# Kernel tuning notes

Measured on AMD Instinct MI355X. Metric: run time of the kernel, lower is better.

Reference implementation:

```python
import jax, jax.numpy as jnp
import numpy as np

B, T, N, F, D, E = 8, 256, 118, 3, 128, 372
G = B * T  # number of graphs after flattening batch*time


def _gcn(x, src, dst, W, b):
    # x: [G, N, Fin] -> PyG GCNConv: X' = D^-1/2 (A+I) D^-1/2 (X W) + b
    h = x @ W  # [G, N, Fout]
    deg = jnp.ones((N,), h.dtype).at[dst].add(1.0)  # in-degree + self loop
    inv = deg ** -0.5
    norm = inv[src] * inv[dst]  # [E]
    agg = h * (1.0 / deg)[None, :, None]  # self-loop term: inv[i]*inv[i] = 1/deg
    agg = agg.at[:, dst].add(h[:, src] * norm[None, :, None])
    return agg + b


def _lstm_layer(x, Wih, Whh, bih, bhh):
    # x: [B, T, I]; PyTorch gate order i, f, g, o
    Bb, H = x.shape[0], Whh.shape[1]
    h0 = jnp.zeros((Bb, H), x.dtype)
    c0 = jnp.zeros((Bb, H), x.dtype)

    def step(carry, xt):
        h, c = carry
        gates = xt @ Wih.T + h @ Whh.T + bih + bhh
        i, f, g, o = jnp.split(gates, 4, axis=-1)
        c = jax.nn.sigmoid(f) * c + jax.nn.sigmoid(i) * jnp.tanh(g)
        h = jax.nn.sigmoid(o) * jnp.tanh(c)
        return (h, c), h

    _, ys = jax.lax.scan(step, (h0, c0), jnp.swapaxes(x, 0, 1))
    return jnp.swapaxes(ys, 0, 1)


def setup_inputs() -> dict:
    key = jax.random.key(0)
    ks = jax.random.split(key, 24)
    s = 0.05

    def rn(i, shape):
        return jax.random.normal(ks[i], shape, jnp.float32) * s

    return {
        "snapshot_sequence": jax.random.normal(ks[0], (B, T, N, F), jnp.float32),
        "edge_index": jax.random.randint(ks[1], (2, E), 0, N, dtype=jnp.int64),
        "scale": jnp.ones((F,), jnp.float32),
        "shift": jnp.zeros((F,), jnp.float32),
        "W1": rn(2, (F, D)), "b1": jnp.zeros((D,), jnp.float32),
        "W2": rn(3, (D, D)), "b2": jnp.zeros((D,), jnp.float32),
        "W3": rn(4, (D, D)), "b3": jnp.zeros((D,), jnp.float32),
        "Wih0": rn(5, (4 * D, D)), "Whh0": rn(6, (4 * D, D)),
        "bih0": jnp.zeros((4 * D,), jnp.float32), "bhh0": jnp.zeros((4 * D,), jnp.float32),
        "Wih1": rn(7, (4 * D, D)), "Whh1": rn(8, (4 * D, D)),
        "bih1": jnp.zeros((4 * D,), jnp.float32), "bhh1": jnp.zeros((4 * D,), jnp.float32),
        "hW1": rn(9, (D, 128)), "hb1": jnp.zeros((128,), jnp.float32),
        "hW2": rn(10, (128, 64)), "hb2": jnp.zeros((64,), jnp.float32),
        "hW3": rn(11, (64, 2)), "hb3": jnp.zeros((2,), jnp.float32),
    }


def reference(snapshot_sequence, edge_index, scale, shift,
              W1, b1, W2, b2, W3, b3,
              Wih0, Whh0, bih0, bhh0, Wih1, Whh1, bih1, bhh1,
              hW1, hb1, hW2, hb2, hW3, hb3):
    src, dst = edge_index[0], edge_index[1]
    x = snapshot_sequence * scale + shift              # FeatureNormalizer
    x = x.reshape(G, N, F)                             # flatten batch*time graphs
    x = jax.nn.silu(_gcn(x, src, dst, W1, b1))         # GCNConv 1 (dropout = eval identity)
    x = jax.nn.silu(_gcn(x, src, dst, W2, b2))         # GCNConv 2
    x = jax.nn.silu(_gcn(x, src, dst, W3, b3))         # GCNConv 3
    emb = x.mean(axis=1)                               # global_mean_pool -> [G, D]
    emb = emb.reshape(B, T, D)
    h = _lstm_layer(emb, Wih0, Whh0, bih0, bhh0)       # 2-layer LSTM (eval: no dropout)
    h = _lstm_layer(h, Wih1, Whh1, bih1, bhh1)
    final = h[:, -1, :]                                # [B, D]
    y = jax.nn.silu(final @ hW1 + hb1)
    y = jax.nn.silu(y @ hW2 + hb2)
    y = y @ hW3 + hb3
    return jax.nn.softplus(y) + 1e-6                   # [B, 2]
```

## Files before the change

### kernel.cpp

```cpp
#include <hip/hip_runtime.h>
#include <math.h>

#define NN 118
#define EE 372
#define GG 2048
#define DD 128
#define TT 256
#define BB 8
#define FD 512

#define XS 136
#define MS 264

typedef short bf16x8 __attribute__((ext_vector_type(8)));
typedef float f32x4  __attribute__((ext_vector_type(4)));
typedef _Float16 f16x2 __attribute__((ext_vector_type(2)));

__device__ __forceinline__ float frcp_(float x) { return __builtin_amdgcn_rcpf(x); }
__device__ __forceinline__ float sig_f(float x) { return frcp_(1.0f + __expf(-x)); }
__device__ __forceinline__ float tanh_f(float x) { return 1.0f - 2.0f * frcp_(__expf(2.0f * x) + 1.0f); }
__device__ __forceinline__ float silu_f(float x) { return x * frcp_(1.0f + __expf(-x)); }
__device__ __forceinline__ float siluf_(float x) { return x / (1.0f + expf(-x)); }

__device__ __forceinline__ float fdot2_(unsigned int a, unsigned int b, float c) {
#if defined(__has_builtin) && __has_builtin(__builtin_amdgcn_fdot2)
    return __builtin_amdgcn_fdot2(__builtin_bit_cast(f16x2, a),
                                  __builtin_bit_cast(f16x2, b), c, false);
#else
    f16x2 x = __builtin_bit_cast(f16x2, a), y = __builtin_bit_cast(f16x2, b);
    return c + (float)x[0] * (float)y[0] + (float)x[1] * (float)y[1];
#endif
}

__device__ __forceinline__ void bar_lds() {
    asm volatile("s_waitcnt lgkmcnt(0)\n\ts_barrier" ::: "memory");
}

__device__ __forceinline__ unsigned short f2bf(float x) {
    unsigned int u = __float_as_uint(x);
    unsigned int r = (u + 0x7fffu + ((u >> 16) & 1u)) >> 16;
    return (unsigned short)r;
}
__device__ __forceinline__ float bf2f(unsigned short b) {
    return __uint_as_float(((unsigned int)b) << 16);
}

__global__ void prep_kernel(const int* __restrict__ ei,
                            const float* __restrict__ bih0, const float* __restrict__ bhh0,
                            const float* __restrict__ bih1, const float* __restrict__ bhh1,
                            float* __restrict__ bias0, float* __restrict__ bias1,
                            unsigned short* __restrict__ AbG) {
    __shared__ int sflag;
    __shared__ int ssrc[EE], sdst[EE];
    __shared__ int scount[NN];
    __shared__ float sinv[NN];
    __shared__ float Adense[NN * NN];
    int tid = threadIdx.x;
    if (tid == 0) sflag = 0;
    __syncthreads();
    for (int i = tid; i < 2 * EE; i += blockDim.x)
        if ((i & 1) && ei[i] != 0) atomicOr(&sflag, 1);
    __syncthreads();
    bool m64 = (sflag == 0);
    for (int e = tid; e < EE; e += blockDim.x) {
        int s, d;
        if (m64) { s = ei[2 * e]; d = ei[2 * EE + 2 * e]; }
        else     { s = ei[e];     d = ei[EE + e]; }
        s = min(max(s, 0), NN - 1); d = min(max(d, 0), NN - 1);
        ssrc[e] = s; sdst[e] = d;
    }
    for (int n = tid; n < NN; n += blockDim.x) scount[n] = 0;
    for (int i = tid; i < NN * NN; i += blockDim.x) Adense[i] = 0.0f;
    __syncthreads();
    for (int e = tid; e < EE; e += blockDim.x) atomicAdd(&scount[sdst[e]], 1);
    __syncthreads();
    for (int n = tid; n < NN; n += blockDim.x) {
        float deg = 1.0f + (float)scount[n];
        sinv[n] = rsqrtf(deg);
        Adense[n * NN + n] = 1.0f / deg;
    }
    __syncthreads();
    for (int e = tid; e < EE; e += blockDim.x)
        atomicAdd(&Adense[sdst[e] * NN + ssrc[e]], sinv[ssrc[e]] * sinv[sdst[e]]);
    __syncthreads();
    for (int i = tid; i < 128 * 128; i += blockDim.x) {
        int r = i >> 7, c = i & 127;
        AbG[i] = (r < NN && c < NN) ? f2bf(Adense[r * NN + c]) : (unsigned short)0;
    }
    for (int j = tid; j < FD; j += blockDim.x) {
        bias0[j] = bih0[j] + bhh0[j];
        bias1[j] = bih1[j] + bhh1[j];
    }
}

__global__ void convw_kernel(const float* __restrict__ W, unsigned short* __restrict__ out) {
    int i = blockIdx.x * 512 + threadIdx.x;
    int n = i >> 7, k = i & 127;
    out[i] = f2bf(W[k * DD + n]);
}

__global__ void convh_kernel(const float* __restrict__ W, unsigned int* __restrict__ out) {
    int i = blockIdx.x * 512 + threadIdx.x;
    int d = i & 127;
    int rest = i >> 7;
    int quarter = rest & 3;
    int qg = rest >> 2;
    int q = qg & 15, g = qg >> 4;
    const float* row = W + (size_t)(g * 128 + d) * 128 + quarter * 32;
    float a = row[2 * q], b = row[2 * q + 1];
    unsigned short lo = __builtin_bit_cast(unsigned short, (_Float16)a);
    unsigned short hi = __builtin_bit_cast(unsigned short, (_Float16)b);
    out[i] = (unsigned int)lo | ((unsigned int)hi << 16);
}

__global__ void transpose_kernel(const float* __restrict__ in, float* __restrict__ out) {
    int idx = blockIdx.x * blockDim.x + threadIdx.x;
    int j = idx >> 7, k = idx & 127;
    out[k * FD + j] = in[idx];
}

__device__ __forceinline__ void mm_agg2(const unsigned short* __restrict__ AbG,
                                        const unsigned short* __restrict__ hS2,
                                        unsigned short* __restrict__ xb2,
                                        const float* __restrict__ bias,
                                        int gr, int wm, int wn, int lm, int lq) {
    f32x4 acc[4][4];
#pragma unroll
    for (int mt = 0; mt < 4; ++mt)
#pragma unroll
        for (int nt = 0; nt < 4; ++nt) acc[mt][nt] = (f32x4){0.f, 0.f, 0.f, 0.f};
#pragma unroll
    for (int kb = 0; kb < 4; ++kb) {
        int ko = kb * 32 + lq * 8;
        bf16x8 bfr[4];
#pragma unroll
        for (int nt = 0; nt < 4; ++nt)
            bfr[nt] = *(const bf16x8*)(hS2 + (wn + nt * 16 + lm) * MS + gr * 128 + ko);
#pragma unroll
        for (int mt = 0; mt < 4; ++mt) {
            bf16x8 af = *(const bf16x8*)(AbG + (wm + mt * 16 + lm) * 128 + ko);
#pragma unroll
            for (int nt = 0; nt < 4; ++nt)
                acc[mt][nt] = __builtin_amdgcn_mfma_f32_16x16x32_bf16(af, bfr[nt], acc[mt][nt], 0, 0, 0);
        }
    }
#pragma unroll
    for (int nt = 0; nt < 4; ++nt) {
        float bn = bias[wn + nt * 16 + lm];
        int col = wn + nt * 16 + lm;
#pragma unroll
        for (int mt = 0; mt < 4; ++mt)
#pragma unroll
            for (int i = 0; i < 4; ++i) {
                float v = silu_f(acc[mt][nt][i] + bn);
                xb2[(gr * 128 + wm + mt * 16 + lq * 4 + i) * XS + col] = f2bf(v);
            }
    }
}

__device__ __forceinline__ void mm_xw2(const unsigned short* __restrict__ xb2,
                                       const unsigned short* __restrict__ WtG,
                                       unsigned short* __restrict__ hS2,
                                       int gr, int wm, int wn, int lm, int lq) {
    f32x4 acc[4][4];
#pragma unroll
    for (int mt = 0; mt < 4; ++mt)
#pragma unroll
        for (int nt = 0; nt < 4; ++nt) acc[mt][nt] = (f32x4){0.f, 0.f, 0.f, 0.f};
#pragma unroll
    for (int kb = 0; kb < 4; ++kb) {
        int ko = kb * 32 + lq * 8;
        bf16x8 bfr[4];
#pragma unroll
        for (int nt = 0; nt < 4; ++nt)
            bfr[nt] = *(const bf16x8*)(WtG + (wn + nt * 16 + lm) * 128 + ko);
#pragma unroll
        for (int mt = 0; mt < 4; ++mt) {
            bf16x8 af = *(const bf16x8*)(xb2 + (gr * 128 + wm + mt * 16 + lm) * XS + ko);
#pragma unroll
            for (int nt = 0; nt < 4; ++nt)
                acc[mt][nt] = __builtin_amdgcn_mfma_f32_16x16x32_bf16(af, bfr[nt], acc[mt][nt], 0, 0, 0);
        }
    }
#pragma unroll
    for (int nt = 0; nt < 4; ++nt)
#pragma unroll
        for (int mt = 0; mt < 4; ++mt) {
            f32x4 a = acc[mt][nt];
            ushort4 pk;
            pk.x = f2bf(a[0]); pk.y = f2bf(a[1]); pk.z = f2bf(a[2]); pk.w = f2bf(a[3]);
            *(ushort4*)(hS2 + (wn + nt * 16 + lm) * MS + gr * 128 + wm + mt * 16 + lq * 4) = pk;
        }
}

__global__ __launch_bounds__(512, 2) void gcn_kernel(
    const float* __restrict__ xg, const float* __restrict__ scale, const float* __restrict__ shift,
    const float* __restrict__ W1, const float* __restrict__ b1,
    const float* __restrict__ b2, const float* __restrict__ b3,
    const unsigned short* __restrict__ AbG,
    const unsigned short* __restrict__ Wt2g, const unsigned short* __restrict__ Wt3g,
    float* __restrict__ emb) {
    extern __shared__ char smem[];
    unsigned short* xb2 = (unsigned short*)smem;
    unsigned short* hS2 = (unsigned short*)(smem + 69632);
    float* xin2  = (float*)(smem + 137216);
    float* meanS = (float*)(smem + 140048);
    int tid = threadIdx.x;
    int lane = tid & 63, w = tid >> 6;
    int gr = w >> 2;
    int wl = w & 3;
    int lm = lane & 15, lq = lane >> 4;
    int wm = (wl & 1) * 64, wn = (wl >> 1) * 64;
    int g0 = blockIdx.x * 2;

    for (int i = tid; i < 4224; i += 512) ((uint4*)hS2)[i] = (uint4){0, 0, 0, 0};
    for (int i = tid; i < 2 * 10 * 64; i += 512) {
        int grr = i >= 640;
        int ii = i - grr * 640;
        int r = grr * 128 + NN + (ii >> 6), c = (ii & 63) * 2;
        *(unsigned int*)(xb2 + r * XS + c) = 0u;
    }
    float s0 = scale[0], s1 = scale[1], s2 = scale[2];
    float t0 = shift[0], t1 = shift[1], t2 = shift[2];
    for (int i = tid; i < 2 * NN * 3; i += 512) {
        int gi = (i >= NN * 3) ? 1 : 0;
        int idx = i - gi * (NN * 3);
        int f = idx % 3;
        float sc = (f == 0) ? s0 : ((f == 1) ? s1 : s2);
        float sf = (f == 0) ? t0 : ((f == 1) ? t1 : t2);
        xin2[gi * 354 + idx] = xg[(size_t)(g0 + gi) * (NN * 3) + idx] * sc + sf;
    }
    int dd = lane * 2;
    float2 w10 = *(const float2*)(W1 + dd);
    float2 w11 = *(const float2*)(W1 + DD + dd);
    float2 w12 = *(const float2*)(W1 + 2 * DD + dd);
    bar_lds();
    const float* xin = xin2 + gr * 354;
    for (int k = 0; k < 30; ++k) {
        int n = wl + 4 * k;
        if (n >= NN) break;
        float x0 = xin[n * 3], x1 = xin[n * 3 + 1], x2 = xin[n * 3 + 2];
        hS2[dd * MS + gr * 128 + n]       = f2bf(x0 * w10.x + x1 * w11.x + x2 * w12.x);
        hS2[(dd + 1) * MS + gr * 128 + n] = f2bf(x0 * w10.y + x1 * w11.y + x2 * w12.y);
    }
    bar_lds();
    mm_agg2(AbG, hS2, xb2, b1, gr, wm, wn, lm, lq);
    bar_lds();
    mm_xw2(xb2, Wt2g, hS2, gr, wm, wn, lm, lq);
    bar_lds();
    mm_agg2(AbG, hS2, xb2, b2, gr, wm, wn, lm, lq);
    bar_lds();
    mm_xw2(xb2, Wt3g, hS2, gr, wm, wn, lm, lq);
    bar_lds();
    mm_agg2(AbG, hS2, xb2, b3, gr, wm, wn, lm, lq);
    bar_lds();
    {
        int grr = tid >> 8, t2 = tid & 255;
        int part = t2 >> 7, d = t2 & 127;
        int a0 = part * 59, a1 = a0 + 59;
        float s = 0.f;
        for (int n = a0; n < a1; ++n) s += bf2f(xb2[(grr * 128 + n) * XS + d]);
        meanS[grr * 256 + part * 128 + d] = s;
    }
    bar_lds();
    if (tid < 256) {
        int grr = tid >> 7, d = tid & 127;
        float s = meanS[grr * 256 + d] + meanS[grr * 256 + 128 + d];
        emb[(size_t)(g0 + grr) * DD + d] = s * (1.0f / (float)NN);
    }
}

__global__ __launch_bounds__(512) void proj_kernel(const float* __restrict__ src,
                                                   const float* __restrict__ WT,
                                                   const float* __restrict__ bias,
                                                   float* __restrict__ dst) {
    __shared__ __align__(16) float eL[DD];
    int g = blockIdx.x, tid = threadIdx.x;
    if (tid < DD) eL[tid] = src[(size_t)g * DD + tid];
    __syncthreads();
    float acc = bias[tid];
    const float* wt = WT + tid;
#pragma unroll 8
    for (int k = 0; k < DD; ++k) acc += eL[k] * wt[(size_t)k * FD];
    dst[(size_t)g * FD + tid] = acc;
}

__global__ __launch_bounds__(512, 2) void scan_kernel(
    const float* __restrict__ inp,
    const unsigned int* __restrict__ Wc,
    float* __restrict__ hout, int full) {
    __shared__ __align__(16) unsigned short hL[DD];
    __shared__ __align__(16) float sgP[3 * DD * 4];
    int b = blockIdx.x, j = threadIdx.x;
    int d = j & 127, quarter = j >> 7;
    unsigned int wreg[4][16];
#pragma unroll
    for (int g = 0; g < 4; ++g)
#pragma unroll
        for (int q = 0; q < 16; ++q)
            wreg[g][q] = Wc[(((g * 16 + q) << 2) + quarter) * 128 + d];
#pragma unroll
    for (int g = 0; g < 4; ++g)
#pragma unroll
        for (int q = 0; q < 16; ++q)
            asm volatile("" : "+v"(wreg[g][q]));
    if (j < 64) ((unsigned int*)hL)[j] = 0u;
    float creg = 0.f;
    const float* ib = inp + (size_t)b * TT * FD;
    float* hb_ = hout + (size_t)b * (full ? TT * DD : DD);
    float xg0[4], xg1[4];
    if (quarter == 0) {
#pragma unroll
        for (int g = 0; g < 4; ++g) { xg0[g] = ib[g * DD + d]; xg1[g] = ib[FD + g * DD + d]; }
    }
    bar_lds();
    for (int t = 0; t < TT; ++t) {
        float xg2[4];
        if (quarter == 0) {
            bool more = (t + 2 < TT);
#pragma unroll
            for (int g = 0; g < 4; ++g)
                xg2[g] = more ? ib[(t + 2) * FD + g * DD + d] : 0.f;
        }
        const uint4* h4 = (const uint4*)(hL + quarter * 32);
        float a0 = 0.f, a1 = 0.f, a2 = 0.f, a3 = 0.f;
#pragma unroll
        for (int c = 0; c < 4; ++c) {
            uint4 hv = h4[c];
            a0 = fdot2_(wreg[0][4 * c + 0], hv.x, a0);
            a1 = fdot2_(wreg[1][4 * c + 0], hv.x, a1);
            a2 = fdot2_(wreg[2][4 * c + 0], hv.x, a2);
            a3 = fdot2_(wreg[3][4 * c + 0], hv.x, a3);
            a0 = fdot2_(wreg[0][4 * c + 1], hv.y, a0);
            a1 = fdot2_(wreg[1][4 * c + 1], hv.y, a1);
            a2 = fdot2_(wreg[2][4 * c + 1], hv.y, a2);
            a3 = fdot2_(wreg[3][4 * c + 1], hv.y, a3);
            a0 = fdot2_(wreg[0][4 * c + 2], hv.z, a0);
            a1 = fdot2_(wreg[1][4 * c + 2], hv.z, a1);
            a2 = fdot2_(wreg[2][4 * c + 2], hv.z, a2);
            a3 = fdot2_(wreg[3][4 * c + 2], hv.z, a3);
            a0 = fdot2_(wreg[0][4 * c + 3], hv.w, a0);
            a1 = fdot2_(wreg[1][4 * c + 3], hv.w, a1);
            a2 = fdot2_(wreg[2][4 * c + 3], hv.w, a2);
            a3 = fdot2_(wreg[3][4 * c + 3], hv.w, a3);
        }
        if (quarter != 0)
            *(float4*)(sgP + ((quarter - 1) * DD + d) * 4) = make_float4(a0, a1, a2, a3);
        bar_lds();
        if (quarter == 0) {
            float4 p1 = *(const float4*)(sgP + d * 4);
            float4 p2 = *(const float4*)(sgP + (DD + d) * 4);
            float4 p3 = *(const float4*)(sgP + (2 * DD + d) * 4);
            float iv = sig_f(a0 + p1.x + p2.x + p3.x + xg0[0]);
            float fv = sig_f(a1 + p1.y + p2.y + p3.y + xg0[1]);
            float gv = tanh_f(a2 + p1.z + p2.z + p3.z + xg0[2]);
            float ov = sig_f(a3 + p1.w + p2.w + p3.w + xg0[3]);
            float cn = fv * creg + iv * gv;
            creg = cn;
            float hn = ov * tanh_f(cn);
            ((_Float16*)hL)[d] = (_Float16)hn;
            if (full) hb_[t * DD + d] = hn;
            else if (t == TT - 1) hb_[d] = hn;
#pragma unroll
            for (int g = 0; g < 4; ++g) { xg0[g] = xg1[g]; xg1[g] = xg2[g]; }
        }
        bar_lds();
    }
}

__global__ void head_kernel(const float* __restrict__ hfin,
                            const float* __restrict__ hW1, const float* __restrict__ hb1,
                            const float* __restrict__ hW2, const float* __restrict__ hb2,
                            const float* __restrict__ hW3, const float* __restrict__ hb3,
                            float* __restrict__ out) {
    __shared__ float fh[BB * DD];
    __shared__ float y1[BB * DD];
    __shared__ float y2[BB * 64];
    int tid = threadIdx.x;
    for (int i = tid; i < BB * DD; i += 256) fh[i] = hfin[i];
    __syncthreads();
    for (int i = tid; i < BB * DD; i += 256) {
        int bb = i >> 7, jj = i & 127;
        float acc = hb1[jj];
        for (int k = 0; k < DD; ++k) acc += fh[(bb << 7) + k] * hW1[(k << 7) + jj];
        y1[i] = siluf_(acc);
    }
    __syncthreads();
    for (int i = tid; i < BB * 64; i += 256) {
        int bb = i >> 6, jj = i & 63;
        float acc = hb2[jj];
        for (int k = 0; k < DD; ++k) acc += y1[(bb << 7) + k] * hW2[(k << 6) + jj];
        y2[i] = siluf_(acc);
    }
    __syncthreads();
    if (tid < BB * 2) {
        int bb = tid >> 1, m = tid & 1;
        float acc = hb3[m];
        for (int k = 0; k < 64; ++k) acc += y2[(bb << 6) + k] * hW3[k * 2 + m];
        float sp = fmaxf(acc, 0.f) + log1pf(expf(-fabsf(acc)));
        out[tid] = sp + 1e-6f;
    }
}

extern "C" void kernel_launch(void* const* d_in, const int* in_sizes, int n_in,
                              void* d_out, int out_size, void* d_ws, size_t ws_size,
                              hipStream_t stream) {
    const float* snap  = (const float*)d_in[0];
    const int*   edges = (const int*)d_in[1];
    const float* scale = (const float*)d_in[2];
    const float* shift = (const float*)d_in[3];
    const float* W1 = (const float*)d_in[4];
    const float* b1 = (const float*)d_in[5];
    const float* W2 = (const float*)d_in[6];
    const float* b2 = (const float*)d_in[7];
    const float* W3 = (const float*)d_in[8];
    const float* b3 = (const float*)d_in[9];
    const float* Wih0 = (const float*)d_in[10];
    const float* Whh0 = (const float*)d_in[11];
    const float* bih0 = (const float*)d_in[12];
    const float* bhh0 = (const float*)d_in[13];
    const float* Wih1 = (const float*)d_in[14];
    const float* Whh1 = (const float*)d_in[15];
    const float* bih1 = (const float*)d_in[16];
    const float* bhh1 = (const float*)d_in[17];
    const float* hW1 = (const float*)d_in[18];
    const float* hb1 = (const float*)d_in[19];
    const float* hW2 = (const float*)d_in[20];
    const float* hb2 = (const float*)d_in[21];
    const float* hW3 = (const float*)d_in[22];
    const float* hb3 = (const float*)d_in[23];

    float* ws = (float*)d_ws;
    float* bias0 = ws + 0;
    float* bias1 = ws + 512;
    unsigned short* AbG  = (unsigned short*)(ws + 1024);
    unsigned short* Wt2g = (unsigned short*)(ws + 9216);
    unsigned short* Wt3g = (unsigned short*)(ws + 17408);
    float* WT0 = ws + 25600;
    float* WT1 = ws + 91136;
    unsigned int* Wc0 = (unsigned int*)(ws + 156672);
    unsigned int* Wc1 = (unsigned int*)(ws + 189440);
    float* emb   = ws + 222208;
    float* inp   = ws + 484352;
    float* h0seq = ws + 1532928;
    float* hfin  = ws + 1795072;

    const int smem_gcn = 142096;
    hipFuncSetAttribute((const void*)gcn_kernel,
                        hipFuncAttributeMaxDynamicSharedMemorySize, smem_gcn);

    prep_kernel<<<1, 256, 0, stream>>>(edges, bih0, bhh0, bih1, bhh1,
                                       bias0, bias1, AbG);
    convw_kernel<<<32, 512, 0, stream>>>(W2, Wt2g);
    convw_kernel<<<32, 512, 0, stream>>>(W3, Wt3g);
    convh_kernel<<<64, 512, 0, stream>>>(Whh0, Wc0);
    convh_kernel<<<64, 512, 0, stream>>>(Whh1, Wc1);
    transpose_kernel<<<128, 512, 0, stream>>>(Wih0, WT0);
    transpose_kernel<<<128, 512, 0, stream>>>(Wih1, WT1);
    gcn_kernel<<<GG / 2, 512, smem_gcn, stream>>>(snap, scale, shift, W1, b1, b2, b3,
                                                  AbG, Wt2g, Wt3g, emb);
    proj_kernel<<<GG, 512, 0, stream>>>(emb, WT0, bias0, inp);
    scan_kernel<<<BB, 512, 0, stream>>>(inp, Wc0, h0seq, 1);
    proj_kernel<<<GG, 512, 0, stream>>>(h0seq, WT1, bias1, inp);
    scan_kernel<<<BB, 512, 0, stream>>>(inp, Wc1, hfin, 0);
    head_kernel<<<1, 256, 0, stream>>>(hfin, hW1, hb1, hW2, hb2, hW3, hb3, (float*)d_out);
}
```

Measured before the change: 604.0 us.

## Fuse both LSTM layers into one wavefront-pipelined scan kernel

```diff
diff --git a/kernel.cpp b/kernel.cpp
--- a/kernel.cpp
+++ b/kernel.cpp
@@ -43,6 +43,11 @@
 }
 __device__ __forceinline__ float bf2f(unsigned short b) {
     return __uint_as_float(((unsigned int)b) << 16);
+}
+__device__ __forceinline__ unsigned int packf16(float a, float b) {
+    unsigned short lo = __builtin_bit_cast(unsigned short, (_Float16)a);
+    unsigned short hi = __builtin_bit_cast(unsigned short, (_Float16)b);
+    return (unsigned int)lo | ((unsigned int)hi << 16);
 }
 
 __global__ void prep_kernel(const int* __restrict__ ei,
@@ -93,30 +98,51 @@
     }
 }
 
-__global__ void convw_kernel(const float* __restrict__ W, unsigned short* __restrict__ out) {
-    int i = blockIdx.x * 512 + threadIdx.x;
-    int n = i >> 7, k = i & 127;
-    out[i] = f2bf(W[k * DD + n]);
-}
-
-__global__ void convh_kernel(const float* __restrict__ W, unsigned int* __restrict__ out) {
-    int i = blockIdx.x * 512 + threadIdx.x;
-    int d = i & 127;
-    int rest = i >> 7;
-    int quarter = rest & 3;
-    int qg = rest >> 2;
-    int q = qg & 15, g = qg >> 4;
-    const float* row = W + (size_t)(g * 128 + d) * 128 + quarter * 32;
-    float a = row[2 * q], b = row[2 * q + 1];
-    unsigned short lo = __builtin_bit_cast(unsigned short, (_Float16)a);
-    unsigned short hi = __builtin_bit_cast(unsigned short, (_Float16)b);
-    out[i] = (unsigned int)lo | ((unsigned int)hi << 16);
-}
-
-__global__ void transpose_kernel(const float* __restrict__ in, float* __restrict__ out) {
-    int idx = blockIdx.x * blockDim.x + threadIdx.x;
-    int j = idx >> 7, k = idx & 127;
-    out[k * FD + j] = in[idx];
+__global__ void convall_kernel(const float* __restrict__ W2, const float* __restrict__ W3,
+                               const float* __restrict__ Whh0,
+                               const float* __restrict__ Wih1, const float* __restrict__ Whh1,
+                               const float* __restrict__ Wih0,
+                               unsigned short* __restrict__ Wt2g, unsigned short* __restrict__ Wt3g,
+                               unsigned int* __restrict__ Wc0, unsigned int* __restrict__ Wc1,
+                               float* __restrict__ WT0) {
+    int bid = blockIdx.x, tid = threadIdx.x;
+    if (bid < 64) {
+        const float* W = (bid < 32) ? W2 : W3;
+        unsigned short* out = (bid < 32) ? Wt2g : Wt3g;
+        int i = (bid & 31) * 512 + tid;
+        int n = i >> 7, k = i & 127;
+        out[i] = f2bf(W[k * DD + n]);
+    } else if (bid < 128) {
+        int i = (bid - 64) * 512 + tid;
+        int d = i & 127;
+        int rest = i >> 7;
+        int quarter = rest & 3;
+        int qg = rest >> 2;
+        int q = qg & 15, g = qg >> 4;
+        const float* row = Whh0 + (size_t)(g * 128 + d) * 128 + quarter * 32;
+        Wc0[i] = packf16(row[2 * q], row[2 * q + 1]);
+    } else if (bid < 256) {
+        int i = (bid - 128) * 512 + tid;
+        int d = i & 127;
+        int rest = i >> 7;
+        int quarter = rest & 3;
+        int qg = rest >> 2;
+        int q = qg & 31, g = qg >> 5;
+        int kk = quarter * 64 + 2 * q;
+        float a, b;
+        if (kk < 128) {
+            const float* row = Wih1 + (size_t)(g * 128 + d) * 128;
+            a = row[kk]; b = row[kk + 1];
+        } else {
+            const float* row = Whh1 + (size_t)(g * 128 + d) * 128;
+            a = row[kk - 128]; b = row[kk - 127];
+        }
+        Wc1[i] = packf16(a, b);
+    } else {
+        int idx = (bid - 256) * 512 + tid;
+        int j = idx >> 7, k = idx & 127;
+        WT0[k * FD + j] = Wih0[idx];
+    }
 }
 
 __device__ __forceinline__ void mm_agg2(const unsigned short* __restrict__ AbG,
@@ -285,36 +311,50 @@
     dst[(size_t)g * FD + tid] = acc;
 }
 
-__global__ __launch_bounds__(512, 2) void scan_kernel(
-    const float* __restrict__ inp,
-    const unsigned int* __restrict__ Wc,
-    float* __restrict__ hout, int full) {
-    __shared__ __align__(16) unsigned short hL[DD];
-    __shared__ __align__(16) float sgP[3 * DD * 4];
+__global__ __launch_bounds__(512, 2) void scan2_kernel(
+    const float* __restrict__ inp0,
+    const unsigned int* __restrict__ Wc0,
+    const unsigned int* __restrict__ Wc1,
+    const float* __restrict__ bias1,
+    float* __restrict__ hfin) {
+    __shared__ __align__(16) unsigned short hcat[256];
+    __shared__ __align__(16) float sgP0[3 * DD * 4];
+    __shared__ __align__(16) float sgP1[3 * DD * 4];
     int b = blockIdx.x, j = threadIdx.x;
     int d = j & 127, quarter = j >> 7;
-    unsigned int wreg[4][16];
+    unsigned int w0[4][16], w1[4][32];
 #pragma unroll
     for (int g = 0; g < 4; ++g)
 #pragma unroll
         for (int q = 0; q < 16; ++q)
-            wreg[g][q] = Wc[(((g * 16 + q) << 2) + quarter) * 128 + d];
+            w0[g][q] = Wc0[(((g * 16 + q) << 2) + quarter) * 128 + d];
 #pragma unroll
     for (int g = 0; g < 4; ++g)
 #pragma unroll
-        for (int q = 0; q < 16; ++q)
-            asm volatile("" : "+v"(wreg[g][q]));
-    if (j < 64) ((unsigned int*)hL)[j] = 0u;
-    float creg = 0.f;
-    const float* ib = inp + (size_t)b * TT * FD;
-    float* hb_ = hout + (size_t)b * (full ? TT * DD : DD);
+        for (int q = 0; q < 32; ++q)
+            w1[g][q] = Wc1[(((g * 32 + q) << 2) + quarter) * 128 + d];
+#pragma unroll
+    for (int g = 0; g < 4; ++g) {
+#pragma unroll
+        for (int q = 0; q < 16; ++q) asm volatile("" : "+v"(w0[g][q]));
+#pragma unroll
+        for (int q = 0; q < 32; ++q) asm volatile("" : "+v"(w1[g][q]));
+    }
+    if (j < 128) ((unsigned int*)hcat)[j] = 0u;
+    float c0 = 0.f, c1 = 0.f;
+    const float* ib = inp0 + (size_t)b * TT * FD;
+    float b1r[4];
     float xg0[4], xg1[4];
     if (quarter == 0) {
 #pragma unroll
-        for (int g = 0; g < 4; ++g) { xg0[g] = ib[g * DD + d]; xg1[g] = ib[FD + g * DD + d]; }
-    }
-    bar_lds();
-    for (int t = 0; t < TT; ++t) {
+        for (int g = 0; g < 4; ++g) {
+            b1r[g] = bias1[g * DD + d];
+            xg0[g] = ib[g * DD + d];
+            xg1[g] = ib[FD + g * DD + d];
+        }
+    }
+    bar_lds();
+    for (int t = 0; t <= TT; ++t) {
         float xg2[4];
         if (quarter == 0) {
             bool more = (t + 2 < TT);
@@ -322,45 +362,66 @@
             for (int g = 0; g < 4; ++g)
                 xg2[g] = more ? ib[(t + 2) * FD + g * DD + d] : 0.f;
         }
-        const uint4* h4 = (const uint4*)(hL + quarter * 32);
+        const uint4* h0q = (const uint4*)(hcat + quarter * 32);
         float a0 = 0.f, a1 = 0.f, a2 = 0.f, a3 = 0.f;
 #pragma unroll
         for (int c = 0; c < 4; ++c) {
-            uint4 hv = h4[c];
-            a0 = fdot2_(wreg[0][4 * c + 0], hv.x, a0);
-            a1 = fdot2_(wreg[1][4 * c + 0], hv.x, a1);
-            a2 = fdot2_(wreg[2][4 * c + 0], hv.x, a2);
-            a3 = fdot2_(wreg[3][4 * c + 0], hv.x, a3);
-            a0 = fdot2_(wreg[0][4 * c + 1], hv.y, a0);
-            a1 = fdot2_(wreg[1][4 * c + 1], hv.y, a1);
-            a2 = fdot2_(wreg[2][4 * c + 1], hv.y, a2);
-            a3 = fdot2_(wreg[3][4 * c + 1], hv.y, a3);
-            a0 = fdot2_(wreg[0][4 * c + 2], hv.z, a0);
-            a1 = fdot2_(wreg[1][4 * c + 2], hv.z, a1);
-            a2 = fdot2_(wreg[2][4 * c + 2], hv.z, a2);
-            a3 = fdot2_(wreg[3][4 * c + 2], hv.z, a3);
-            a0 = fdot2_(wreg[0][4 * c + 3], hv.w, a0);
-            a1 = fdot2_(wreg[1][4 * c + 3], hv.w, a1);
-            a2 = fdot2_(wreg[2][4 * c + 3], hv.w, a2);
-            a3 = fdot2_(wreg[3][4 * c + 3], hv.w, a3);
-        }
-        if (quarter != 0)
-            *(float4*)(sgP + ((quarter - 1) * DD + d) * 4) = make_float4(a0, a1, a2, a3);
+            uint4 hv = h0q[c];
+            a0 = fdot2_(w0[0][4 * c + 0], hv.x, a0); a1 = fdot2_(w0[1][4 * c + 0], hv.x, a1);
+            a2 = fdot2_(w0[2][4 * c + 0], hv.x, a2); a3 = fdot2_(w0[3][4 * c + 0], hv.x, a3);
+            a0 = fdot2_(w0[0][4 * c + 1], hv.y, a0); a1 = fdot2_(w0[1][4 * c + 1], hv.y, a1);
+            a2 = fdot2_(w0[2][4 * c + 1], hv.y, a2); a3 = fdot2_(w0[3][4 * c + 1], hv.y, a3);
+            a0 = fdot2_(w0[0][4 * c + 2], hv.z, a0); a1 = fdot2_(w0[1][4 * c + 2], hv.z, a1);
+            a2 = fdot2_(w0[2][4 * c + 2], hv.z, a2); a3 = fdot2_(w0[3][4 * c + 2], hv.z, a3);
+            a0 = fdot2_(w0[0][4 * c + 3], hv.w, a0); a1 = fdot2_(w0[1][4 * c + 3], hv.w, a1);
+            a2 = fdot2_(w0[2][4 * c + 3], hv.w, a2); a3 = fdot2_(w0[3][4 * c + 3], hv.w, a3);
+        }
+        const uint4* h1q = (const uint4*)(hcat + quarter * 64);
+        float e0 = 0.f, e1 = 0.f, e2 = 0.f, e3 = 0.f;
+#pragma unroll
+        for (int c = 0; c < 8; ++c) {
+            uint4 hv = h1q[c];
+            e0 = fdot2_(w1[0][4 * c + 0], hv.x, e0); e1 = fdot2_(w1[1][4 * c + 0], hv.x, e1);
+            e2 = fdot2_(w1[2][4 * c + 0], hv.x, e2); e3 = fdot2_(w1[3][4 * c + 0], hv.x, e3);
+            e0 = fdot2_(w1[0][4 * c + 1], hv.y, e0); e1 = fdot2_(w1[1][4 * c + 1], hv.y, e1);
+            e2 = fdot2_(w1[2][4 * c + 1], hv.y, e2); e3 = fdot2_(w1[3][4 * c + 1], hv.y, e3);
+            e0 = fdot2_(w1[0][4 * c + 2], hv.z, e0); e1 = fdot2_(w1[1][4 * c + 2], hv.z, e1);
+            e2 = fdot2_(w1[2][4 * c + 2], hv.z, e2); e3 = fdot2_(w1[3][4 * c + 2], hv.z, e3);
+            e0 = fdot2_(w1[0][4 * c + 3], hv.w, e0); e1 = fdot2_(w1[1][4 * c + 3], hv.w, e1);
+            e2 = fdot2_(w1[2][4 * c + 3], hv.w, e2); e3 = fdot2_(w1[3][4 * c + 3], hv.w, e3);
+        }
+        if (quarter != 0) {
+            *(float4*)(sgP0 + ((quarter - 1) * DD + d) * 4) = make_float4(a0, a1, a2, a3);
+            *(float4*)(sgP1 + ((quarter - 1) * DD + d) * 4) = make_float4(e0, e1, e2, e3);
+        }
         bar_lds();
         if (quarter == 0) {
-            float4 p1 = *(const float4*)(sgP + d * 4);
-            float4 p2 = *(const float4*)(sgP + (DD + d) * 4);
-            float4 p3 = *(const float4*)(sgP + (2 * DD + d) * 4);
-            float iv = sig_f(a0 + p1.x + p2.x + p3.x + xg0[0]);
-            float fv = sig_f(a1 + p1.y + p2.y + p3.y + xg0[1]);
-            float gv = tanh_f(a2 + p1.z + p2.z + p3.z + xg0[2]);
-            float ov = sig_f(a3 + p1.w + p2.w + p3.w + xg0[3]);
-            float cn = fv * creg + iv * gv;
-            creg = cn;
-            float hn = ov * tanh_f(cn);
-            ((_Float16*)hL)[d] = (_Float16)hn;
-            if (full) hb_[t * DD + d] = hn;
-            else if (t == TT - 1) hb_[d] = hn;
+            if (t < TT) {
+                float4 p1 = *(const float4*)(sgP0 + d * 4);
+                float4 p2 = *(const float4*)(sgP0 + (DD + d) * 4);
+                float4 p3 = *(const float4*)(sgP0 + (2 * DD + d) * 4);
+                float iv = sig_f(a0 + p1.x + p2.x + p3.x + xg0[0]);
+                float fv = sig_f(a1 + p1.y + p2.y + p3.y + xg0[1]);
+                float gv = tanh_f(a2 + p1.z + p2.z + p3.z + xg0[2]);
+                float ov = sig_f(a3 + p1.w + p2.w + p3.w + xg0[3]);
+                float cn = fv * c0 + iv * gv;
+                c0 = cn;
+                ((_Float16*)hcat)[d] = (_Float16)(ov * tanh_f(cn));
+            }
+            if (t >= 1) {
+                float4 q1 = *(const float4*)(sgP1 + d * 4);
+                float4 q2 = *(const float4*)(sgP1 + (DD + d) * 4);
+                float4 q3 = *(const float4*)(sgP1 + (2 * DD + d) * 4);
+                float iv = sig_f(e0 + q1.x + q2.x + q3.x + b1r[0]);
+                float fv = sig_f(e1 + q1.y + q2.y + q3.y + b1r[1]);
+                float gv = tanh_f(e2 + q1.z + q2.z + q3.z + b1r[2]);
+                float ov = sig_f(e3 + q1.w + q2.w + q3.w + b1r[3]);
+                float cn = fv * c1 + iv * gv;
+                c1 = cn;
+                float hn = ov * tanh_f(cn);
+                ((_Float16*)hcat)[128 + d] = (_Float16)hn;
+                if (t == TT) hfin[b * DD + d] = hn;
+            }
 #pragma unroll
             for (int g = 0; g < 4; ++g) { xg0[g] = xg1[g]; xg1[g] = xg2[g]; }
         }
@@ -437,13 +498,11 @@
     unsigned short* Wt2g = (unsigned short*)(ws + 9216);
     unsigned short* Wt3g = (unsigned short*)(ws + 17408);
     float* WT0 = ws + 25600;
-    float* WT1 = ws + 91136;
-    unsigned int* Wc0 = (unsigned int*)(ws + 156672);
-    unsigned int* Wc1 = (unsigned int*)(ws + 189440);
-    float* emb   = ws + 222208;
-    float* inp   = ws + 484352;
-    float* h0seq = ws + 1532928;
-    float* hfin  = ws + 1795072;
+    unsigned int* Wc0 = (unsigned int*)(ws + 91136);
+    unsigned int* Wc1 = (unsigned int*)(ws + 123904);
+    float* emb  = ws + 189440;
+    float* inp  = ws + 451584;
+    float* hfin = ws + 1500160;
 
     const int smem_gcn = 142096;
     hipFuncSetAttribute((const void*)gcn_kernel,
@@ -451,17 +510,11 @@
 
     prep_kernel<<<1, 256, 0, stream>>>(edges, bih0, bhh0, bih1, bhh1,
                                        bias0, bias1, AbG);
-    convw_kernel<<<32, 512, 0, stream>>>(W2, Wt2g);
-    convw_kernel<<<32, 512, 0, stream>>>(W3, Wt3g);
-    convh_kernel<<<64, 512, 0, stream>>>(Whh0, Wc0);
-    convh_kernel<<<64, 512, 0, stream>>>(Whh1, Wc1);
-    transpose_kernel<<<128, 512, 0, stream>>>(Wih0, WT0);
-    transpose_kernel<<<128, 512, 0, stream>>>(Wih1, WT1);
+    convall_kernel<<<384, 512, 0, stream>>>(W2, W3, Whh0, Wih1, Whh1, Wih0,
+                                            Wt2g, Wt3g, Wc0, Wc1, WT0);
     gcn_kernel<<<GG / 2, 512, smem_gcn, stream>>>(snap, scale, shift, W1, b1, b2, b3,
                                                   AbG, Wt2g, Wt3g, emb);
     proj_kernel<<<GG, 512, 0, stream>>>(emb, WT0, bias0, inp);
-    scan_kernel<<<BB, 512, 0, stream>>>(inp, Wc0, h0seq, 1);
-    proj_kernel<<<GG, 512, 0, stream>>>(h0seq, WT1, bias1, inp);
-    scan_kernel<<<BB, 512, 0, stream>>>(inp, Wc1, hfin, 0);
+    scan2_kernel<<<BB, 512, 0, stream>>>(inp, Wc0, Wc1, bias1, hfin);
     head_kernel<<<1, 256, 0, stream>>>(hfin, hW1, hb1, hW2, hb2, hW3, hb3, (float*)d_out);
 }
```

Result: no change. 607.6 us (+0.6%).
